# Performance work log

Measured on AMD Instinct MI355X. Metric: run time of the kernel, lower is better.

The kernel has to match this reference:

```python
import jax, jax.numpy as jnp
import numpy as np

B, L, DIM = 2, 2048, 2048
N_HEADS, N_KV_HEADS = 32, 8
HEAD_DIM = DIM // N_HEADS  # 64
SCALE = HEAD_DIM ** -0.5


def setup_inputs() -> dict:
    key = jax.random.key(0)
    ks = jax.random.split(key, 6)
    s = 0.02
    x = jax.random.normal(ks[0], (B, L, DIM), dtype=jnp.float32)
    wq = jax.random.normal(ks[1], (N_HEADS * HEAD_DIM, DIM), dtype=jnp.float32) * s
    wk = jax.random.normal(ks[2], (N_KV_HEADS * HEAD_DIM, DIM), dtype=jnp.float32) * s
    wv = jax.random.normal(ks[3], (N_KV_HEADS * HEAD_DIM, DIM), dtype=jnp.float32) * s
    wo = jax.random.normal(ks[4], (DIM, N_HEADS * HEAD_DIM), dtype=jnp.float32) * s
    # standard RoPE frequencies: theta = 10000^(-2i/d), angle = pos * theta
    inv_freq = 1.0 / (10000.0 ** (jnp.arange(0, HEAD_DIM, 2, dtype=jnp.float32) / HEAD_DIM))
    angles = jnp.arange(L, dtype=jnp.float32)[:, None] * inv_freq[None, :]  # [L, HEAD_DIM//2]
    freqs_cos = jnp.cos(angles)
    freqs_sin = jnp.sin(angles)
    # additive causal mask [1, 1, L, L]
    causal = jnp.tril(jnp.ones((L, L), dtype=bool))
    mask = jnp.where(causal, 0.0, -1e9).astype(jnp.float32)[None, None]
    return {"x": x, "wq": wq, "wk": wk, "wv": wv, "wo": wo,
            "freqs_cos": freqs_cos, "freqs_sin": freqs_sin, "mask": mask}


def _apply_rope(t, cos, sin):
    # t: [B, H, L, D]; complex pairing is (even, odd) interleaved along D
    te, to = t[..., 0::2], t[..., 1::2]
    cos = cos[None, None, : t.shape[2], :]
    sin = sin[None, None, : t.shape[2], :]
    re = te * cos - to * sin
    im = te * sin + to * cos
    return jnp.stack([re, im], axis=-1).reshape(t.shape)


def reference(x, wq, wk, wv, wo, freqs_cos, freqs_sin, mask):
    b, l, _ = x.shape
    q = (x @ wq.T).reshape(b, l, N_HEADS, HEAD_DIM).transpose(0, 2, 1, 3)
    k = (x @ wk.T).reshape(b, l, N_KV_HEADS, HEAD_DIM).transpose(0, 2, 1, 3)
    v = (x @ wv.T).reshape(b, l, N_KV_HEADS, HEAD_DIM).transpose(0, 2, 1, 3)
    q = _apply_rope(q, freqs_cos, freqs_sin)
    k = _apply_rope(k, freqs_cos, freqs_sin)
    repeats = N_HEADS // N_KV_HEADS
    k = jnp.repeat(k, repeats, axis=1)
    v = jnp.repeat(v, repeats, axis=1)
    scores = jnp.einsum("bhqd,bhkd->bhqk", q, k) * SCALE + mask
    probs = jax.nn.softmax(scores, axis=-1)
    out = jnp.einsum("bhqk,bhkd->bhqd", probs, v)
    out = out.transpose(0, 2, 1, 3).reshape(b, l, N_HEADS * HEAD_DIM)
    return out @ wo.T
```

## Files before the change

### kernel.cpp

```cpp
#include <hip/hip_runtime.h>
#include <hip/hip_bf16.h>
#include <stdint.h>

typedef __attribute__((ext_vector_type(8))) short bf16x8;
typedef __attribute__((ext_vector_type(4))) float f32x4;
typedef __attribute__((ext_vector_type(16))) float f32x16;
typedef __attribute__((ext_vector_type(4))) unsigned int u32x4;

#define B_    2
#define L_    2048
#define DIM_  2048
#define NH_   32
#define NKV_  8
#define HD_   64
#define KVD_  512
#define CLOG_ 0.1803368801111244f

__device__ __forceinline__ unsigned short f2bf(float f) {
  unsigned u = __float_as_uint(f);
  u += 0x7fff + ((u >> 16) & 1);
  return (unsigned short)(u >> 16);
}
__device__ __forceinline__ unsigned cvtpk(float lo, float hi_) {
  unsigned r;
  asm("v_cvt_pk_bf16_f32 %0, %1, %2" : "=v"(r) : "v"(lo), "v"(hi_));
  return r;
}
__device__ __forceinline__ float bf2f(unsigned short h) {
  return __uint_as_float(((unsigned)h) << 16);
}
__device__ __forceinline__ void plswap2(unsigned &a, unsigned &b, int hi) {
#if __has_builtin(__builtin_amdgcn_permlane32_swap)
  auto r = __builtin_amdgcn_permlane32_swap(a, b, false, false);
  a = (unsigned)r[0]; b = (unsigned)r[1];
#else
  unsigned xa = (unsigned)__shfl_xor((int)a, 32);
  unsigned xb = (unsigned)__shfl_xor((int)b, 32);
  unsigned na = hi ? xb : a, nb = hi ? b : xa;
  a = na; b = nb;
#endif
}

#define GLDS16(gsrc, ldst) __builtin_amdgcn_global_load_lds( \
    (const __attribute__((address_space(1))) unsigned int*)(gsrc), \
    (__attribute__((address_space(3))) unsigned int*)(ldst), 16, 0, 0)

__global__ void cvt_all(const float* __restrict__ x,  const float* __restrict__ wq,
                        const float* __restrict__ wk, const float* __restrict__ wv,
                        const float* __restrict__ wo,
                        unsigned short* __restrict__ xb,  unsigned short* __restrict__ wqb,
                        unsigned short* __restrict__ wkb, unsigned short* __restrict__ wvb,
                        unsigned short* __restrict__ wob) {
  int i = blockIdx.x * blockDim.x + threadIdx.x;
  const float* src; unsigned short* dst; int off;
  if (i < 2097152)      { src = x;  dst = xb;  off = i; }
  else if (i < 3145728) { src = wq; dst = wqb; off = i - 2097152; }
  else if (i < 3407872) { src = wk; dst = wkb; off = i - 3145728; }
  else if (i < 3670016) { src = wv; dst = wvb; off = i - 3407872; }
  else                  { src = wo; dst = wob; off = i - 3670016; }
  float4 v = reinterpret_cast<const float4*>(src)[off];
  ushort4 o;
  o.x = f2bf(v.x); o.y = f2bf(v.y); o.z = f2bf(v.z); o.w = f2bf(v.w);
  reinterpret_cast<ushort4*>(dst)[off] = o;
}

template<int OUTMODE>
__device__ __forceinline__ void gemm128_core(
    const unsigned short* __restrict__ A,
    const unsigned short* __restrict__ W,
    void* __restrict__ C, int N, int K, int m0, int n0,
    unsigned short (*As)[128 * 64], unsigned short (*Bs)[128 * 64])
{
  const int tid = threadIdx.x;
  const int lane = tid & 63, wid = tid >> 6;
  const int wm = wid >> 1, wn = wid & 1;
  const int r = lane & 15, g = lane >> 4;
  const int rsw = (r & 7) << 4;
  f32x4 acc[4][4] = {};

  auto STAGE = [&](int buf, int k0) {
#pragma unroll
    for (int p = 0; p < 4; ++p) {
      int off = (p * 256 + tid) * 16;
      int row = off >> 7;
      int colb = (off & 127) ^ ((row & 7) << 4);
      GLDS16((const char*)A + ((size_t)(m0 + row) * K + k0) * 2 + colb,
             (char*)As[buf] + off);
      GLDS16((const char*)W + ((size_t)(n0 + row) * K + k0) * 2 + colb,
             (char*)Bs[buf] + off);
    }
  };

  const int nt = K >> 6;
  STAGE(0, 0);
  asm volatile("s_waitcnt vmcnt(0)" ::: "memory");
  __builtin_amdgcn_s_barrier();
  int cur = 0;
  for (int kt = 0; kt < nt; ++kt) {
    if (kt + 1 < nt) {
      STAGE(cur ^ 1, (kt + 1) << 6);
      asm volatile("s_waitcnt vmcnt(8)" ::: "memory");
    } else {
      asm volatile("s_waitcnt vmcnt(0)" ::: "memory");
    }
    __builtin_amdgcn_s_barrier();
    __builtin_amdgcn_sched_barrier(0);
    const char* Ab = (const char*)As[cur];
    const char* Bb = (const char*)Bs[cur];
    __builtin_amdgcn_s_setprio(1);
#pragma unroll
    for (int kk = 0; kk < 2; ++kk) {
      bf16x8 af[4], bfv[4];
#pragma unroll
      for (int i = 0; i < 4; ++i)
        af[i] = *reinterpret_cast<const bf16x8*>(
            Ab + (wm * 64 + i * 16 + r) * 128 + ((kk * 64 + g * 16) ^ rsw));
#pragma unroll
      for (int i = 0; i < 4; ++i)
        bfv[i] = *reinterpret_cast<const bf16x8*>(
            Bb + (wn * 64 + i * 16 + r) * 128 + ((kk * 64 + g * 16) ^ rsw));
#pragma unroll
      for (int i = 0; i < 4; ++i)
#pragma unroll
        for (int j = 0; j < 4; ++j)
          acc[i][j] = __builtin_amdgcn_mfma_f32_16x16x32_bf16(af[i], bfv[j], acc[i][j], 0, 0, 0);
    }
    __builtin_amdgcn_s_setprio(0);
    asm volatile("s_waitcnt lgkmcnt(0)" ::: "memory");
    __builtin_amdgcn_s_barrier();
    cur ^= 1;
  }

  if (OUTMODE == 2) {
#pragma unroll
    for (int i = 0; i < 4; ++i)
#pragma unroll
      for (int jf = 0; jf < 4; ++jf) {
        int col = n0 + wn * 64 + jf * 16 + r;
        int kvi = col >> 6, d = col & 63;
        int tok = m0 + wm * 64 + i * 16 + g * 4;
        int bb = tok >> 11, tl = tok & (L_ - 1);
        uint2 u;
        u.x = cvtpk(acc[i][jf][0], acc[i][jf][1]);
        u.y = cvtpk(acc[i][jf][2], acc[i][jf][3]);
        *reinterpret_cast<uint2*>((unsigned short*)C +
            ((size_t)((bb * NKV_ + kvi) * HD_ + d)) * L_ + tl) = u;
      }
  } else {
#pragma unroll
    for (int i = 0; i < 4; ++i)
#pragma unroll
      for (int jf = 0; jf < 4; ++jf)
#pragma unroll
        for (int j = 0; j < 4; ++j) {
          size_t row = (size_t)(m0 + wm * 64 + i * 16 + g * 4 + j);
          size_t col = (size_t)(n0 + wn * 64 + jf * 16 + r);
          float v = acc[i][jf][j];
          if (OUTMODE == 1) ((float*)C)[row * N + col] = v;
          else ((unsigned short*)C)[row * N + col] = f2bf(v);
        }
  }
}

template<int OUT_F32>
__global__ __launch_bounds__(256) void gemm_bt(
    const unsigned short* __restrict__ A,
    const unsigned short* __restrict__ W,
    void* __restrict__ C, int M, int N, int K)
{
  __shared__ unsigned short As[2][128 * 64];
  __shared__ unsigned short Bs[2][128 * 64];
  gemm128_core<OUT_F32 ? 1 : 0>(A, W, C, N, K, blockIdx.y * 128, blockIdx.x * 128, As, Bs);
}

__global__ __launch_bounds__(256) void gemm_qkv(
    const unsigned short* __restrict__ A,
    const unsigned short* __restrict__ Wq,
    const unsigned short* __restrict__ Wk,
    const unsigned short* __restrict__ Wv,
    unsigned short* __restrict__ Cq,
    unsigned short* __restrict__ Ck,
    unsigned short* __restrict__ Vt)
{
  __shared__ unsigned short As[2][128 * 64];
  __shared__ unsigned short Bs[2][128 * 64];
  const int bx = blockIdx.x;
  const int m0 = blockIdx.y * 128;
  if (bx < 16)
    gemm128_core<0>(A, Wq, Cq, 2048, DIM_, m0, bx * 128, As, Bs);
  else if (bx < 20)
    gemm128_core<0>(A, Wk, Ck, 512, DIM_, m0, (bx - 16) * 128, As, Bs);
  else
    gemm128_core<2>(A, Wv, Vt, 512, DIM_, m0, (bx - 20) * 128, As, Bs);
}

__global__ void rope_v8(unsigned short* __restrict__ t,
                        const float* __restrict__ fc,
                        const float* __restrict__ fs,
                        int rowElems, int lshift, float scale) {
  int idx = blockIdx.x * blockDim.x + threadIdx.x;
  int row = idx >> lshift;
  if (row >= B_ * L_) return;
  int pos = (idx & ((1 << lshift) - 1)) << 3;
  int l = row & (L_ - 1);
  int i0 = (pos & 63) >> 1;
  unsigned short* p = t + (size_t)row * rowElems + pos;
  uint4 v = *reinterpret_cast<const uint4*>(p);
  float4 c4 = *reinterpret_cast<const float4*>(fc + l * 32 + i0);
  float4 s4 = *reinterpret_cast<const float4*>(fs + l * 32 + i0);
  float cc[4] = {c4.x * scale, c4.y * scale, c4.z * scale, c4.w * scale};
  float ss[4] = {s4.x * scale, s4.y * scale, s4.z * scale, s4.w * scale};
  unsigned wds[4] = {v.x, v.y, v.z, v.w};
  uint4 o;
  unsigned ow[4];
#pragma unroll
  for (int k = 0; k < 4; ++k) {
    float te = bf2f((unsigned short)(wds[k] & 0xffff));
    float to = bf2f((unsigned short)(wds[k] >> 16));
    ow[k] = cvtpk(te * cc[k] - to * ss[k], te * ss[k] + to * cc[k]);
  }
  o.x = ow[0]; o.y = ow[1]; o.z = ow[2]; o.w = ow[3];
  *reinterpret_cast<uint4*>(p) = o;
}

__global__ __launch_bounds__(256) void attn_kernel(
    const unsigned short* __restrict__ Q,
    const unsigned short* __restrict__ K,
    const unsigned short* __restrict__ Vt,
    unsigned short* __restrict__ AO)
{
  __shared__ unsigned short Ks[2][64 * 64];
  __shared__ unsigned short Vs[2][64 * 64];
  const int tid = threadIdx.x;
  const int lane = tid & 63, w = tid >> 6;
  const int ql = lane & 31;
  const int hi = lane >> 5;
  const int wid = blockIdx.x;
  const int j = wid >> 6;
  const int blk = j >> 2, pos = j & 3;
  const int base = 15 - 4 * blk;
  const int qt = (blk & 1) ? (base - 3 + pos) : (base - pos);
  const int bh = wid & 63;
  const int b = bh >> 5, h = bh & 31, kv = h >> 2;
  const int q0 = qt * 128;
  const int qw = q0 + w * 32;
  const int nkt = (q0 + 128) >> 6;

  bf16x8 qf[4];
  const unsigned short* qbase = Q + ((size_t)(b * L_ + qw + ql)) * DIM_ + h * HD_ + hi * 8;
#pragma unroll
  for (int dk = 0; dk < 4; ++dk)
    qf[dk] = *reinterpret_cast<const bf16x8*>(qbase + dk * 16);

  const unsigned short* Kg = K + (size_t)b * L_ * KVD_ + kv * HD_;
  const unsigned short* Vg = Vt + ((size_t)(b * NKV_ + kv)) * HD_ * L_;

  f32x16 oacc0 = {}, oacc1 = {};
  float lrow = 0.f;
  const int rsw = (ql & 7) << 4;

  auto STAGE = [&](int buf, int t) {
    const int k0 = t * 64;
#pragma unroll
    for (int p = 0; p < 2; ++p) {
      int off = (p * 256 + tid) * 16;
      int row = off >> 7;
      int colb = (off & 127) ^ ((row & 7) << 4);
      GLDS16((const char*)Kg + ((size_t)(k0 + row)) * (KVD_ * 2) + colb,
             (char*)Ks[buf] + off);
      GLDS16((const char*)Vg + ((size_t)row) * (L_ * 2) + (size_t)k0 * 2 + colb,
             (char*)Vs[buf] + off);
    }
  };

  int cur = 0;
  STAGE(0, 0);
  asm volatile("s_waitcnt vmcnt(0)" ::: "memory");
  __builtin_amdgcn_s_barrier();

  for (int t = 0; t < nkt; ++t) {
    if (t + 1 < nkt) {
      STAGE(cur ^ 1, t + 1);
      asm volatile("s_waitcnt vmcnt(4)" ::: "memory");
    } else {
      asm volatile("s_waitcnt vmcnt(0)" ::: "memory");
    }
    __builtin_amdgcn_s_barrier();
    __builtin_amdgcn_sched_barrier(0);
    const int k0 = t * 64;
    if (k0 < qw + 32) {
      const char* Kl = (const char*)Ks[cur];
      const char* Vl = (const char*)Vs[cur];
      f32x16 s0 = {}, s1 = {};
      __builtin_amdgcn_s_setprio(1);
#pragma unroll
      for (int dk = 0; dk < 4; ++dk) {
        bf16x8 kf0 = *reinterpret_cast<const bf16x8*>(Kl + ql * 128 + ((dk * 32 + hi * 16) ^ rsw));
        bf16x8 kf1 = *reinterpret_cast<const bf16x8*>(Kl + (32 + ql) * 128 + ((dk * 32 + hi * 16) ^ rsw));
        s0 = __builtin_amdgcn_mfma_f32_32x32x16_bf16(kf0, qf[dk], s0, 0, 0, 0);
        s1 = __builtin_amdgcn_mfma_f32_32x32x16_bf16(kf1, qf[dk], s1, 0, 0, 0);
      }
      __builtin_amdgcn_s_setprio(0);
      float p[32];
      float ps = 0.f;
      if (k0 + 63 > qw) {
        int q = qw + ql;
#pragma unroll
        for (int i = 0; i < 32; ++i) {
          float sv = (i < 16) ? s0[i] : s1[i - 16];
          int kk = k0 + (i >> 4) * 32 + (i & 3) + 8 * ((i & 15) >> 2) + 4 * hi;
          float e = exp2f(sv);
          e = (kk > q) ? 0.f : e;
          p[i] = e; ps += e;
        }
      } else {
#pragma unroll
        for (int i = 0; i < 32; ++i) {
          float sv = (i < 16) ? s0[i] : s1[i - 16];
          p[i] = exp2f(sv); ps += p[i];
        }
      }
      lrow += ps;
      bf16x8 pf[4];
#pragma unroll
      for (int s = 0; s < 4; ++s) {
        int bp = ((s >> 1) << 4) + ((s & 1) << 3);
        unsigned w0 = cvtpk(p[bp + 0], p[bp + 1]);
        unsigned w1 = cvtpk(p[bp + 2], p[bp + 3]);
        unsigned w2 = cvtpk(p[bp + 4], p[bp + 5]);
        unsigned w3 = cvtpk(p[bp + 6], p[bp + 7]);
        plswap2(w0, w2, hi);
        plswap2(w1, w3, hi);
        u32x4 fw;
        fw[0] = w0; fw[1] = w1; fw[2] = w2; fw[3] = w3;
        pf[s] = __builtin_bit_cast(bf16x8, fw);
      }
      __builtin_amdgcn_s_setprio(1);
#pragma unroll
      for (int s = 0; s < 4; ++s) {
        bf16x8 v0 = *reinterpret_cast<const bf16x8*>(Vl + ql * 128 + ((s * 32 + hi * 16) ^ rsw));
        bf16x8 v1 = *reinterpret_cast<const bf16x8*>(Vl + (32 + ql) * 128 + ((s * 32 + hi * 16) ^ rsw));
        oacc0 = __builtin_amdgcn_mfma_f32_32x32x16_bf16(v0, pf[s], oacc0, 0, 0, 0);
        oacc1 = __builtin_amdgcn_mfma_f32_32x32x16_bf16(v1, pf[s], oacc1, 0, 0, 0);
      }
      __builtin_amdgcn_s_setprio(0);
    }
    asm volatile("s_waitcnt lgkmcnt(0)" ::: "memory");
    __builtin_amdgcn_s_barrier();
    cur ^= 1;
  }

  unsigned la = __float_as_uint(lrow), lb = __float_as_uint(lrow);
  plswap2(la, lb, hi);
  float ltot = __uint_as_float(la) + __uint_as_float(lb);
  float inv = 1.f / ltot;
  unsigned short* obase = AO + ((size_t)(b * L_ + qw + ql)) * DIM_ + h * HD_;
#pragma unroll
  for (int g4 = 0; g4 < 4; ++g4) {
    uint2 u;
    u.x = cvtpk(oacc0[g4 * 4 + 0] * inv, oacc0[g4 * 4 + 1] * inv);
    u.y = cvtpk(oacc0[g4 * 4 + 2] * inv, oacc0[g4 * 4 + 3] * inv);
    *reinterpret_cast<uint2*>(obase + g4 * 8 + hi * 4) = u;
    uint2 v;
    v.x = cvtpk(oacc1[g4 * 4 + 0] * inv, oacc1[g4 * 4 + 1] * inv);
    v.y = cvtpk(oacc1[g4 * 4 + 2] * inv, oacc1[g4 * 4 + 3] * inv);
    *reinterpret_cast<uint2*>(obase + 32 + g4 * 8 + hi * 4) = v;
  }
}

extern "C" void kernel_launch(void* const* d_in, const int* in_sizes, int n_in,
                              void* d_out, int out_size, void* d_ws, size_t ws_size,
                              hipStream_t stream) {
  const float* x  = (const float*)d_in[0];
  const float* wq = (const float*)d_in[1];
  const float* wk = (const float*)d_in[2];
  const float* wv = (const float*)d_in[3];
  const float* wo = (const float*)d_in[4];
  const float* fc = (const float*)d_in[5];
  const float* fs = (const float*)d_in[6];
  float* out = (float*)d_out;

  unsigned short* ws  = (unsigned short*)d_ws;
  unsigned short* xb  = ws;
  unsigned short* wqb = xb  + 8388608;
  unsigned short* wkb = wqb + 4194304;
  unsigned short* wvb = wkb + 1048576;
  unsigned short* wob = wvb + 1048576;
  unsigned short* Qb  = wob + 4194304;
  unsigned short* Kb  = Qb  + 8388608;
  unsigned short* Vtb = Kb  + 2097152;
  unsigned short* AOb = Vtb + 2097152;

  cvt_all<<<18432, 256, 0, stream>>>(x, wq, wk, wv, wo, xb, wqb, wkb, wvb, wob);

  gemm_qkv<<<dim3(24, 32), 256, 0, stream>>>(xb, wqb, wkb, wvb, Qb, Kb, Vtb);

  rope_v8<<<4096, 256, 0, stream>>>(Qb, fc, fs, 2048, 8, CLOG_);
  rope_v8<<<1024, 256, 0, stream>>>(Kb, fc, fs, 512, 6, 1.0f);

  attn_kernel<<<1024, 256, 0, stream>>>(Qb, Kb, Vtb, AOb);

  gemm_bt<1><<<dim3(16, 32), 256, 0, stream>>>(AOb, wob, out, 4096, 2048, 2048);
}
```

Baseline: 221.3 us.

## Switch projection GEMMs to 256x256 tiles with 512-thread blocks

Both the QKV projection GEMM and the output projection GEMM move from 128x128 tiles on 256 threads to 256x256 tiles on 512 threads (8 waves, each computing 128x64). The inner loop is reordered to preload B fragments once per k-tile and stream A fragments in pairs, with setprio around each MFMA group. The goal is higher arithmetic intensity and fewer global and LDS loads per FLOP. The cost is 128 KB of LDS per block, a larger accumulator register footprint, and far fewer blocks (192 and 128) against 256 CUs, which risks under-filling the GPU.

Measured after the change: 238.8 us. 7.9% more time.

```diff
diff --git a/kernel.cpp b/kernel.cpp
--- a/kernel.cpp
+++ b/kernel.cpp
@@ -65,23 +65,23 @@
 }
 
 template<int OUTMODE>
-__device__ __forceinline__ void gemm128_core(
+__device__ __forceinline__ void gemm256_core(
     const unsigned short* __restrict__ A,
     const unsigned short* __restrict__ W,
     void* __restrict__ C, int N, int K, int m0, int n0,
-    unsigned short (*As)[128 * 64], unsigned short (*Bs)[128 * 64])
+    unsigned short (*As)[256 * 64], unsigned short (*Bs)[256 * 64])
 {
   const int tid = threadIdx.x;
   const int lane = tid & 63, wid = tid >> 6;
-  const int wm = wid >> 1, wn = wid & 1;
+  const int wm = wid >> 2, wn = wid & 3;
   const int r = lane & 15, g = lane >> 4;
   const int rsw = (r & 7) << 4;
-  f32x4 acc[4][4] = {};
+  f32x4 acc[8][4] = {};
 
   auto STAGE = [&](int buf, int k0) {
 #pragma unroll
     for (int p = 0; p < 4; ++p) {
-      int off = (p * 256 + tid) * 16;
+      int off = (p * 512 + tid) * 16;
       int row = off >> 7;
       int colb = (off & 127) ^ ((row & 7) << 4);
       GLDS16((const char*)A + ((size_t)(m0 + row) * K + k0) * 2 + colb,
@@ -107,25 +107,33 @@
     __builtin_amdgcn_sched_barrier(0);
     const char* Ab = (const char*)As[cur];
     const char* Bb = (const char*)Bs[cur];
-    __builtin_amdgcn_s_setprio(1);
-#pragma unroll
-    for (int kk = 0; kk < 2; ++kk) {
-      bf16x8 af[4], bfv[4];
-#pragma unroll
-      for (int i = 0; i < 4; ++i)
-        af[i] = *reinterpret_cast<const bf16x8*>(
-            Ab + (wm * 64 + i * 16 + r) * 128 + ((kk * 64 + g * 16) ^ rsw));
-#pragma unroll
-      for (int i = 0; i < 4; ++i)
-        bfv[i] = *reinterpret_cast<const bf16x8*>(
-            Bb + (wn * 64 + i * 16 + r) * 128 + ((kk * 64 + g * 16) ^ rsw));
-#pragma unroll
-      for (int i = 0; i < 4; ++i)
-#pragma unroll
-        for (int j = 0; j < 4; ++j)
-          acc[i][j] = __builtin_amdgcn_mfma_f32_16x16x32_bf16(af[i], bfv[j], acc[i][j], 0, 0, 0);
-    }
-    __builtin_amdgcn_s_setprio(0);
+    bf16x8 bfv[4][2];
+#pragma unroll
+    for (int ni = 0; ni < 4; ++ni)
+#pragma unroll
+      for (int kk = 0; kk < 2; ++kk)
+        bfv[ni][kk] = *reinterpret_cast<const bf16x8*>(
+            Bb + (wn * 64 + ni * 16 + r) * 128 + ((kk * 64 + g * 16) ^ rsw));
+#pragma unroll
+    for (int p = 0; p < 4; ++p) {
+      bf16x8 af[2][2];
+#pragma unroll
+      for (int mi = 0; mi < 2; ++mi)
+#pragma unroll
+        for (int kk = 0; kk < 2; ++kk)
+          af[mi][kk] = *reinterpret_cast<const bf16x8*>(
+              Ab + (wm * 128 + (p * 2 + mi) * 16 + r) * 128 + ((kk * 64 + g * 16) ^ rsw));
+      __builtin_amdgcn_s_setprio(1);
+#pragma unroll
+      for (int mi = 0; mi < 2; ++mi)
+#pragma unroll
+        for (int ni = 0; ni < 4; ++ni)
+#pragma unroll
+          for (int kk = 0; kk < 2; ++kk)
+            acc[p * 2 + mi][ni] = __builtin_amdgcn_mfma_f32_16x16x32_bf16(
+                af[mi][kk], bfv[ni][kk], acc[p * 2 + mi][ni], 0, 0, 0);
+      __builtin_amdgcn_s_setprio(0);
+    }
     asm volatile("s_waitcnt lgkmcnt(0)" ::: "memory");
     __builtin_amdgcn_s_barrier();
     cur ^= 1;
@@ -133,47 +141,36 @@
 
   if (OUTMODE == 2) {
 #pragma unroll
-    for (int i = 0; i < 4; ++i)
-#pragma unroll
-      for (int jf = 0; jf < 4; ++jf) {
-        int col = n0 + wn * 64 + jf * 16 + r;
+    for (int mi = 0; mi < 8; ++mi)
+#pragma unroll
+      for (int ni = 0; ni < 4; ++ni) {
+        int col = n0 + wn * 64 + ni * 16 + r;
         int kvi = col >> 6, d = col & 63;
-        int tok = m0 + wm * 64 + i * 16 + g * 4;
+        int tok = m0 + wm * 128 + mi * 16 + g * 4;
         int bb = tok >> 11, tl = tok & (L_ - 1);
         uint2 u;
-        u.x = cvtpk(acc[i][jf][0], acc[i][jf][1]);
-        u.y = cvtpk(acc[i][jf][2], acc[i][jf][3]);
+        u.x = cvtpk(acc[mi][ni][0], acc[mi][ni][1]);
+        u.y = cvtpk(acc[mi][ni][2], acc[mi][ni][3]);
         *reinterpret_cast<uint2*>((unsigned short*)C +
             ((size_t)((bb * NKV_ + kvi) * HD_ + d)) * L_ + tl) = u;
       }
   } else {
 #pragma unroll
-    for (int i = 0; i < 4; ++i)
-#pragma unroll
-      for (int jf = 0; jf < 4; ++jf)
+    for (int mi = 0; mi < 8; ++mi)
+#pragma unroll
+      for (int ni = 0; ni < 4; ++ni)
 #pragma unroll
         for (int j = 0; j < 4; ++j) {
-          size_t row = (size_t)(m0 + wm * 64 + i * 16 + g * 4 + j);
-          size_t col = (size_t)(n0 + wn * 64 + jf * 16 + r);
-          float v = acc[i][jf][j];
+          size_t row = (size_t)(m0 + wm * 128 + mi * 16 + g * 4 + j);
+          size_t col = (size_t)(n0 + wn * 64 + ni * 16 + r);
+          float v = acc[mi][ni][j];
           if (OUTMODE == 1) ((float*)C)[row * N + col] = v;
           else ((unsigned short*)C)[row * N + col] = f2bf(v);
         }
   }
 }
 
-template<int OUT_F32>
-__global__ __launch_bounds__(256) void gemm_bt(
-    const unsigned short* __restrict__ A,
-    const unsigned short* __restrict__ W,
-    void* __restrict__ C, int M, int N, int K)
-{
-  __shared__ unsigned short As[2][128 * 64];
-  __shared__ unsigned short Bs[2][128 * 64];
-  gemm128_core<OUT_F32 ? 1 : 0>(A, W, C, N, K, blockIdx.y * 128, blockIdx.x * 128, As, Bs);
-}
-
-__global__ __launch_bounds__(256) void gemm_qkv(
+__global__ __launch_bounds__(512, 2) void gemm_qkv256(
     const unsigned short* __restrict__ A,
     const unsigned short* __restrict__ Wq,
     const unsigned short* __restrict__ Wk,
@@ -182,16 +179,26 @@
     unsigned short* __restrict__ Ck,
     unsigned short* __restrict__ Vt)
 {
-  __shared__ unsigned short As[2][128 * 64];
-  __shared__ unsigned short Bs[2][128 * 64];
+  __shared__ unsigned short As[2][256 * 64];
+  __shared__ unsigned short Bs[2][256 * 64];
   const int bx = blockIdx.x;
-  const int m0 = blockIdx.y * 128;
-  if (bx < 16)
-    gemm128_core<0>(A, Wq, Cq, 2048, DIM_, m0, bx * 128, As, Bs);
-  else if (bx < 20)
-    gemm128_core<0>(A, Wk, Ck, 512, DIM_, m0, (bx - 16) * 128, As, Bs);
+  const int m0 = blockIdx.y * 256;
+  if (bx < 8)
+    gemm256_core<0>(A, Wq, Cq, 2048, DIM_, m0, bx * 256, As, Bs);
+  else if (bx < 10)
+    gemm256_core<0>(A, Wk, Ck, 512, DIM_, m0, (bx - 8) * 256, As, Bs);
   else
-    gemm128_core<2>(A, Wv, Vt, 512, DIM_, m0, (bx - 20) * 128, As, Bs);
+    gemm256_core<2>(A, Wv, Vt, 512, DIM_, m0, (bx - 10) * 256, As, Bs);
+}
+
+__global__ __launch_bounds__(512, 2) void gemm_out256(
+    const unsigned short* __restrict__ A,
+    const unsigned short* __restrict__ W,
+    float* __restrict__ C)
+{
+  __shared__ unsigned short As[2][256 * 64];
+  __shared__ unsigned short Bs[2][256 * 64];
+  gemm256_core<1>(A, W, C, DIM_, DIM_, blockIdx.y * 256, blockIdx.x * 256, As, Bs);
 }
 
 __global__ void rope_v8(unsigned short* __restrict__ t,
@@ -393,12 +400,12 @@
 
   cvt_all<<<18432, 256, 0, stream>>>(x, wq, wk, wv, wo, xb, wqb, wkb, wvb, wob);
 
-  gemm_qkv<<<dim3(24, 32), 256, 0, stream>>>(xb, wqb, wkb, wvb, Qb, Kb, Vtb);
+  gemm_qkv256<<<dim3(12, 16), 512, 0, stream>>>(xb, wqb, wkb, wvb, Qb, Kb, Vtb);
 
   rope_v8<<<4096, 256, 0, stream>>>(Qb, fc, fs, 2048, 8, CLOG_);
   rope_v8<<<1024, 256, 0, stream>>>(Kb, fc, fs, 512, 6, 1.0f);
 
   attn_kernel<<<1024, 256, 0, stream>>>(Qb, Kb, Vtb, AOb);
 
-  gemm_bt<1><<<dim3(16, 32), 256, 0, stream>>>(AOb, wob, out, 4096, 2048, 2048);
-}
+  gemm_out256<<<dim3(8, 16), 512, 0, stream>>>(AOb, wob, out);
+}
```
